# Kernel tuning notes

Hardware: AMD Instinct MI355X
Metric: run time of the kernel (lower is better)

## Reference

```python
import jax, jax.numpy as jnp
import numpy as np

H = 128
NH = 8  # num attention heads


def _ln(x, g, b, eps=1e-5):
    m = x.mean(-1, keepdims=True)
    v = ((x - m) ** 2).mean(-1, keepdims=True)
    return (x - m) / jnp.sqrt(v + eps) * g + b


def _mha(q_in, kv_in, Wqkv, bqkv, Wo, bo):
    # torch nn.MultiheadAttention with packed in_proj, batch=1, eval (no dropout)
    h = q_in.shape[-1]
    hd = h // NH
    Wq, Wk, Wv = Wqkv[:h], Wqkv[h:2 * h], Wqkv[2 * h:]
    bq, bk, bv = bqkv[:h], bqkv[h:2 * h], bqkv[2 * h:]
    q = (q_in @ Wq.T + bq).reshape(-1, NH, hd).transpose(1, 0, 2)   # [nh, Nq, hd]
    k = (kv_in @ Wk.T + bk).reshape(-1, NH, hd).transpose(1, 0, 2)  # [nh, Nk, hd]
    v = (kv_in @ Wv.T + bv).reshape(-1, NH, hd).transpose(1, 0, 2)
    scores = jnp.einsum('hqd,hkd->hqk', q, k) / jnp.sqrt(jnp.asarray(hd, q.dtype))
    attn = jax.nn.softmax(scores, axis=-1)
    out = jnp.einsum('hqk,hkd->hqd', attn, v)                       # [nh, Nq, hd]
    out = out.transpose(1, 0, 2).reshape(-1, h)
    return out @ Wo.T + bo


def setup_inputs() -> dict:
    key = jax.random.key(0)
    ks = jax.random.split(key, 32)
    s = 0.05
    d = {
        'ligand_features': jax.random.normal(ks[0], (512, 128), jnp.float32),
        'pocket_features': jax.random.normal(ks[1], (1024, 128), jnp.float32),
        'ligand_coords': jax.random.uniform(ks[2], (512, 3), jnp.float32) * 20.0,
        'pocket_coords': jax.random.uniform(ks[3], (1024, 3), jnp.float32) * 20.0,
        # projections
        'Wl': jax.random.normal(ks[4], (H, 128), jnp.float32) * s,
        'bl': jnp.zeros((H,), jnp.float32),
        'Wp': jax.random.normal(ks[5], (H, 128), jnp.float32) * s,
        'bp': jnp.zeros((H,), jnp.float32),
        # distance encoder: 1 -> h/4 -> h/2 -> h
        'Wd1': jax.random.normal(ks[6], (H // 4, 1), jnp.float32) * s,
        'bd1': jnp.zeros((H // 4,), jnp.float32),
        'Wd2': jax.random.normal(ks[7], (H // 2, H // 4), jnp.float32) * s,
        'bd2': jnp.zeros((H // 2,), jnp.float32),
        'Wd3': jax.random.normal(ks[8], (H, H // 2), jnp.float32) * s,
        'bd3': jnp.zeros((H,), jnp.float32),
        # gates
        'Wgl': jax.random.normal(ks[9], (H, 2 * H), jnp.float32) * s,
        'bgl': jnp.zeros((H,), jnp.float32),
        'Wgp': jax.random.normal(ks[10], (H, 2 * H), jnp.float32) * s,
        'bgp': jnp.zeros((H,), jnp.float32),
        # shared cross-attention (packed qkv like torch)
        'Wqkv': jax.random.normal(ks[11], (3 * H, H), jnp.float32) * s,
        'bqkv': jnp.zeros((3 * H,), jnp.float32),
        'Wo': jax.random.normal(ks[12], (H, H), jnp.float32) * s,
        'bo': jnp.zeros((H,), jnp.float32),
        # layer norms
        'g_l': jnp.ones((H,), jnp.float32),
        'be_l': jnp.zeros((H,), jnp.float32),
        'g_p': jnp.ones((H,), jnp.float32),
        'be_p': jnp.zeros((H,), jnp.float32),
    }
    return d


def reference(ligand_features, pocket_features, ligand_coords, pocket_coords,
              Wl, bl, Wp, bp, Wd1, bd1, Wd2, bd2, Wd3, bd3,
              Wgl, bgl, Wgp, bgp, Wqkv, bqkv, Wo, bo,
              g_l, be_l, g_p, be_p):
    lig = ligand_features @ Wl.T + bl   # [Nl, H]
    poc = pocket_features @ Wp.T + bp   # [Np, H]

    # pairwise distances [Nl, Np]
    diff = ligand_coords[:, None, :] - pocket_coords[None, :, :]
    dist = jnp.sqrt(jnp.sum(diff * diff, axis=-1))

    # distance encoder MLP applied elementwise -> [Nl, Np, H]
    e = jax.nn.relu(dist[..., None] @ Wd1.T + bd1)
    e = jax.nn.relu(e @ Wd2.T + bd2)
    enc = e @ Wd3.T + bd3
    m = enc.mean(axis=-1)               # [Nl, Np]

    # ligand enhancement: softmax over pocket axis
    sw_l = jax.nn.softmax(-m, axis=-1)          # [Nl, Np]
    agg_l = sw_l @ poc                          # [Nl, H]
    gate_l = jax.nn.sigmoid(jnp.concatenate([lig, agg_l], axis=-1) @ Wgl.T + bgl)
    lig_enh = gate_l * lig + (1.0 - gate_l) * agg_l

    # pocket enhancement: transposed encoding, softmax over ligand axis
    sw_p = jax.nn.softmax(-m.T, axis=-1)        # [Np, Nl]
    agg_p = sw_p @ lig                          # [Np, H]
    gate_p = jax.nn.sigmoid(jnp.concatenate([poc, agg_p], axis=-1) @ Wgp.T + bgp)
    poc_enh = gate_p * poc + (1.0 - gate_p) * agg_p

    lig_att = _mha(lig_enh, poc_enh, Wqkv, bqkv, Wo, bo)
    poc_att = _mha(poc_enh, lig_enh, Wqkv, bqkv, Wo, bo)

    lig_fused = _ln(lig_enh + lig_att, g_l, be_l)
    poc_fused = _ln(poc_enh + poc_att, g_p, be_p)
    return (lig_fused, poc_fused)
```

## Files before the change

### kernel.cpp

```cpp
#include <hip/hip_runtime.h>
#include <math.h>

#define NL 512
#define NP 1024
#define HDIM 128

#define TAB_N 8192
#define DMAX 34.65f

#define M_OFF    128
#define WLT_OFF  (M_OFF)
#define WPT_OFF  (M_OFF + 16384)
#define WQT_OFF  (M_OFF + 32768)
#define WOT_OFF  (M_OFF + 81920)
#define WGLT_OFF (M_OFF + 98304)
#define WGPT_OFF (M_OFF + 131072)
#define TAB_OFF  (M_OFF + 163840)
#define LIG_OFF  (M_OFF + NL*NP)
#define POC_OFF  (LIG_OFF + NL*HDIM)
#define LENH_OFF (POC_OFF + NP*HDIM)
#define PENH_OFF (LENH_OFF + NL*HDIM)
#define QKVL_OFF (PENH_OFF + NP*HDIM)
#define QKVP_OFF (QKVL_OFF + NL*384)
#define PARTL_OFF (QKVP_OFF + NP*384)
#define PARTP_OFF (PARTL_OFF + 512*8*8*18)

__device__ __forceinline__ float dot4f(float4 a, float4 b){
  return fmaf(a.x,b.x, fmaf(a.y,b.y, fmaf(a.z,b.z, a.w*b.w)));
}

__device__ __forceinline__ void tpose(const float* __restrict__ src, float* __restrict__ dst,
                                      int O, int K, int blk0, int t){
  int e0 = blk0*1024 + t*4;
  #pragma unroll
  for (int i = 0; i < 4; i++){
    int e = e0 + i;
    int o = e / K, k = e - o*K;
    dst[(size_t)k*O + o] = src[(size_t)o*K + k];
  }
}
__global__ __launch_bounds__(256) void prep_all(const float* __restrict__ Wl, const float* __restrict__ Wp,
                                                const float* __restrict__ Wqkv, const float* __restrict__ Wo,
                                                const float* __restrict__ Wgl, const float* __restrict__ Wgp,
                                                const float* __restrict__ Wd1, const float* __restrict__ bd1,
                                                const float* __restrict__ Wd2, const float* __restrict__ bd2,
                                                const float* __restrict__ Wd3, const float* __restrict__ bd3,
                                                float* __restrict__ ws){
  int b = blockIdx.x, t = threadIdx.x;
  if (b < 160){
    if      (b < 16)  tpose(Wl,   ws + WLT_OFF,  128, 128, b,       t);
    else if (b < 32)  tpose(Wp,   ws + WPT_OFF,  128, 128, b - 16,  t);
    else if (b < 80)  tpose(Wqkv, ws + WQT_OFF,  384, 128, b - 32,  t);
    else if (b < 96)  tpose(Wo,   ws + WOT_OFF,  128, 128, b - 80,  t);
    else if (b < 128) tpose(Wgl,  ws + WGLT_OFF, 128, 256, b - 96,  t);
    else              tpose(Wgp,  ws + WGPT_OFF, 128, 256, b - 128, t);
    return;
  }
  float* tab = ws + TAB_OFF;
  __shared__ float sWd1[32], sbd1[32], sWd2[2048], sbd2[64], swd3m[64];
  __shared__ float sbd3m;
  int idx = (b - 160) * 256 + t;
  if (t < 64){
    float s = 0.f;
    #pragma unroll 8
    for (int i = 0; i < 128; i++) s += Wd3[i*64 + t];
    swd3m[t] = s * (1.f/128.f);
  } else if (t == 64){
    float s = 0.f;
    for (int i = 0; i < 128; i++) s += bd3[i];
    sbd3m = s * (1.f/128.f);
  } else if (t >= 128 && t < 160){ sWd1[t-128] = Wd1[t-128]; sbd1[t-128] = bd1[t-128]; }
  else if (t >= 160 && t < 224){ sbd2[t-160] = bd2[t-160]; }
  for (int k = t; k < 2048; k += 256) sWd2[k] = Wd2[k];
  __syncthreads();

  float d = (float)idx * (DMAX / (float)(TAB_N - 1));
  float4 e1q[8];
  const float4* w1q = (const float4*)sWd1;
  const float4* b1q = (const float4*)sbd1;
  #pragma unroll
  for (int k4 = 0; k4 < 8; k4++){
    float4 w = w1q[k4], bb = b1q[k4];
    float4 e;
    e.x = fmaxf(fmaf(d, w.x, bb.x), 0.f);
    e.y = fmaxf(fmaf(d, w.y, bb.y), 0.f);
    e.z = fmaxf(fmaf(d, w.z, bb.z), 0.f);
    e.w = fmaxf(fmaf(d, w.w, bb.w), 0.f);
    e1q[k4] = e;
  }
  float mv = sbd3m;
  #pragma unroll 4
  for (int j2 = 0; j2 < 64; j2++){
    const float4* wrow = (const float4*)(sWd2 + j2*32);
    float a0 = 0.f, a1 = 0.f, a2 = 0.f, a3 = 0.f;
    #pragma unroll
    for (int k4 = 0; k4 < 8; k4++){
      float4 w = wrow[k4], e = e1q[k4];
      a0 = fmaf(w.x, e.x, a0);
      a1 = fmaf(w.y, e.y, a1);
      a2 = fmaf(w.z, e.z, a2);
      a3 = fmaf(w.w, e.w, a3);
    }
    float e2v = fmaxf(sbd2[j2] + ((a0+a1)+(a2+a3)), 0.f);
    mv = fmaf(swd3m[j2], e2v, mv);
  }
  tab[idx] = mv;
}

__global__ __launch_bounds__(1024) void proj_kernel(const float* __restrict__ lf, const float* __restrict__ pf,
                                                    const float* __restrict__ WlT, const float* __restrict__ bl,
                                                    const float* __restrict__ WpT, const float* __restrict__ bp,
                                                    float* __restrict__ lig, float* __restrict__ poc){
  int b = blockIdx.x, t = threadIdx.x;
  bool isLig = (b < 64);
  int r0 = isLig ? b*8 : (b - 64)*8;
  const float* in = (isLig ? lf : pf) + (size_t)r0*HDIM;
  const float* WT = isLig ? WlT : WpT;
  const float* bias = isLig ? bl : bp;
  float* out = (isLig ? lig : poc) + (size_t)r0*HDIM;
  __shared__ float sx[8*HDIM];
  sx[t] = in[t];
  __syncthreads();
  int r = t >> 7, col = t & 127;
  const float* xr = sx + r*HDIM;
  float acc = bias[col];
  #pragma unroll 8
  for (int k = 0; k < 128; k++) acc = fmaf(WT[k*128 + col], xr[k], acc);
  out[r*HDIM + col] = acc;
}

__global__ __launch_bounds__(1024) void agg_gate_fused(const float* __restrict__ lc, const float* __restrict__ pc,
                                                       const float* __restrict__ tab,
                                                       const float* __restrict__ lig, const float* __restrict__ poc,
                                                       const float* __restrict__ WglT, const float* __restrict__ bgl,
                                                       const float* __restrict__ WgpT, const float* __restrict__ bgp,
                                                       const float* __restrict__ WqkvT, const float* __restrict__ bqkv,
                                                       float* __restrict__ lenh, float* __restrict__ penh,
                                                       float* __restrict__ qkvl, float* __restrict__ qkvp){
  int b = blockIdx.x, t = threadIdx.x;
  bool isLig = (b < NL/4);
  int r0 = isLig ? b*4 : (b - NL/4)*4;
  int n = isLig ? NP : NL;
  const float* myFeat = isLig ? lig : poc;
  const float* otherFeat = isLig ? poc : lig;
  const float* myC = isLig ? lc : pc;
  const float* otC = isLig ? pc : lc;

  __shared__ float w[4*NP];
  __shared__ float sx[4*HDIM];
  __shared__ float sa[4*HDIM];
  __shared__ float part[16*512];
  __shared__ float redm[16];
  __shared__ float sgm[4], sinv[4];

  int rr = t >> 8, u = t & 255;
  int lane = t & 63, wv = t >> 6;
  int row = r0 + rr;

  if (t < 512) sx[t] = myFeat[(size_t)r0*HDIM + t];

  float cx = myC[row*3+0], cy = myC[row*3+1], cz = myC[row*3+2];
  const float inv_h = (float)(TAB_N - 1) / DMAX;
  int per = n >> 8;

  float xs[4];
  float lmax = -1e30f;
  for (int k = 0; k < per; k++){
    int j = u + (k << 8);
    float ox = otC[j*3+0], oy = otC[j*3+1], oz = otC[j*3+2];
    float dx = cx-ox, dy = cy-oy, dz = cz-oz;
    float d = sqrtf(fmaf(dx,dx, fmaf(dy,dy, dz*dz)));
    float xf = d * inv_h;
    int i0 = (int)xf;
    i0 = (i0 > TAB_N-2) ? (TAB_N-2) : i0;
    float f = xf - (float)i0;
    float v0 = tab[i0], v1 = tab[i0+1];
    xs[k] = -fmaf(f, v1 - v0, v0);
    lmax = fmaxf(lmax, xs[k]);
  }
  float v = lmax;
  #pragma unroll
  for (int off = 32; off; off >>= 1) v = fmaxf(v, __shfl_down(v, off));
  if (lane == 0) redm[wv] = v;
  __syncthreads();
  if (t < 4) sgm[t] = fmaxf(fmaxf(redm[t*4+0], redm[t*4+1]), fmaxf(redm[t*4+2], redm[t*4+3]));
  __syncthreads();
  float gm = sgm[rr];
  float lsum = 0.f;
  for (int k = 0; k < per; k++){
    float e = __expf(xs[k] - gm);
    w[rr*NP + u + (k << 8)] = e;
    lsum += e;
  }
  v = lsum;
  #pragma unroll
  for (int off = 32; off; off >>= 1) v += __shfl_down(v, off);
  if (lane == 0) redm[wv] = v;
  __syncthreads();
  if (t < 4) sinv[t] = 1.0f / ((redm[t*4+0] + redm[t*4+1]) + (redm[t*4+2] + redm[t*4+3]));
  __syncthreads();

  {
    int jg = t >> 6;
    int rp = (t >> 5) & 1;
    int c4 = t & 31;
    int per2 = n >> 4;
    int jb0 = jg * per2;
    int rA = rp*2, rB = rp*2 + 1;
    const float4* of4 = (const float4*)otherFeat;
    const float* wA = w + rA*NP;
    const float* wB = w + rB*NP;
    float4 accA = {0,0,0,0}, accB = {0,0,0,0};
    #pragma unroll 4
    for (int jj = 0; jj < per2; jj++){
      int j = jb0 + jj;
      float4 f = of4[(size_t)j*32 + c4];
      float w0 = wA[j], w1 = wB[j];
      accA.x = fmaf(w0, f.x, accA.x); accA.y = fmaf(w0, f.y, accA.y);
      accA.z = fmaf(w0, f.z, accA.z); accA.w = fmaf(w0, f.w, accA.w);
      accB.x = fmaf(w1, f.x, accB.x); accB.y = fmaf(w1, f.y, accB.y);
      accB.z = fmaf(w1, f.z, accB.z); accB.w = fmaf(w1, f.w, accB.w);
    }
    float4* p4 = (float4*)part;
    p4[jg*128 + rA*32 + c4] = accA;
    p4[jg*128 + rB*32 + c4] = accB;
  }
  __syncthreads();
  {
    float4* p4 = (float4*)part;
    #pragma unroll
    for (int s = 8; s >= 1; s >>= 1){
      if (t < s*128){
        int jg2 = t >> 7, rem = t & 127;
        float4 a = p4[jg2*128 + rem], bb = p4[(jg2+s)*128 + rem];
        a.x += bb.x; a.y += bb.y; a.z += bb.z; a.w += bb.w;
        p4[jg2*128 + rem] = a;
      }
      __syncthreads();
    }
  }
  if (t < 512){
    int r = t >> 7;
    sa[t] = part[t] * sinv[r];
  }
  __syncthreads();

  float enh_val = 0.f;
  {
    if (t < 512){
      int r = t >> 7, col = t & 127;
      const float* WT = isLig ? WglT : WgpT;
      const float* bg = isLig ? bgl : bgp;
      const float* xr = sx + r*HDIM;
      const float* ar = sa + r*HDIM;
      float g = bg[col];
      #pragma unroll 8
      for (int k = 0; k < 128; k++) g = fmaf(WT[k*128 + col], xr[k], g);
      #pragma unroll 8
      for (int k = 0; k < 128; k++) g = fmaf(WT[(128+k)*128 + col], ar[k], g);
      g = 1.0f / (1.0f + __expf(-g));
      float xv = xr[col], av = ar[col];
      enh_val = fmaf(g, xv - av, av);
      float* dst = isLig ? (lenh + (size_t)(r0+r)*HDIM) : (penh + (size_t)(r0+r)*HDIM);
      dst[col] = enh_val;
    }
  }
  __syncthreads();
  if (t < 512) sa[t] = enh_val;
  __syncthreads();

  if (t < 512){
    int r = t >> 7, c0 = t & 127;
    const float* er = sa + r*HDIM;
    float acc0 = bqkv[c0], acc1 = bqkv[c0+128], acc2 = bqkv[c0+256];
    #pragma unroll 4
    for (int k = 0; k < 128; k++){
      float xv = er[k];
      const float* wk = WqkvT + k*384;
      acc0 = fmaf(wk[c0],       xv, acc0);
      acc1 = fmaf(wk[c0+128],   xv, acc1);
      acc2 = fmaf(wk[c0+256],   xv, acc2);
    }
    float* qout = (isLig ? qkvl : qkvp) + (size_t)(r0+r)*384;
    qout[c0] = acc0; qout[c0+128] = acc1; qout[c0+256] = acc2;
  }
}

__global__ __launch_bounds__(256) void attn_part(const float* __restrict__ qkvl, const float* __restrict__ qkvp,
                                                 float* __restrict__ partL, float* __restrict__ partP){
  int bx = blockIdx.x;
  int t = threadIdx.x;
  const float* qsrc; const float* kvsrc; int qt, slice; bool isLig;
  if (bx < 256){ isLig = true;  qt = bx >> 3; slice = bx & 7; qsrc = qkvl; kvsrc = qkvp; }
  else { int b2 = bx - 256; isLig = false; qt = b2 >> 2; slice = b2 & 3; qsrc = qkvp; kvsrc = qkvl; }
  int g = t >> 6, tt = t & 63;
  int h = tt >> 3, qp = tt & 7;
  int j0 = slice*128 + g*32;

  const float4* qA = (const float4*)(qsrc + (size_t)(qt*16+qp)*384 + h*16);
  const float4* qB = (const float4*)(qsrc + (size_t)(qt*16+qp+8)*384 + h*16);
  float4 a0 = qA[0], a1 = qA[1], a2 = qA[2], a3 = qA[3];
  float4 b0 = qB[0], b1 = qB[1], b2 = qB[2], b3 = qB[3];
  float mA = -1e30f, lA = 0.f, mB = -1e30f, lB = 0.f;
  float4 OA0={0,0,0,0}, OA1={0,0,0,0}, OA2={0,0,0,0}, OA3={0,0,0,0};
  float4 OB0={0,0,0,0}, OB1={0,0,0,0}, OB2={0,0,0,0}, OB3={0,0,0,0};

  __shared__ float sKV[8192];
  float* myKV = sKV + g*2048;

  for (int tile = 0; tile < 4; tile++){
    int jbase = j0 + tile*8;
    __syncthreads();
    #pragma unroll
    for (int nn = 0; nn < 8; nn++){
      int v4 = tt + nn*64;
      int jj = v4 >> 6, c4 = v4 & 63;
      ((float4*)myKV)[jj*64 + c4] = *(const float4*)(kvsrc + (size_t)(jbase+jj)*384 + 128 + c4*4);
    }
    __syncthreads();
    float sA[8], sB[8];
    #pragma unroll
    for (int jj = 0; jj < 8; jj++){
      const float4* kk = (const float4*)(myKV + jj*256 + h*16);
      float4 k0 = kk[0], k1 = kk[1], k2 = kk[2], k3 = kk[3];
      sA[jj] = (dot4f(a0,k0) + dot4f(a1,k1) + dot4f(a2,k2) + dot4f(a3,k3)) * 0.25f;
      sB[jj] = (dot4f(b0,k0) + dot4f(b1,k1) + dot4f(b2,k2) + dot4f(b3,k3)) * 0.25f;
    }
    float mtA = sA[0], mtB = sB[0];
    #pragma unroll
    for (int jj = 1; jj < 8; jj++){ mtA = fmaxf(mtA, sA[jj]); mtB = fmaxf(mtB, sB[jj]); }
    float mnA = fmaxf(mA, mtA), mnB = fmaxf(mB, mtB);
    float cA = __expf(mA - mnA), cB = __expf(mB - mnB);
    lA *= cA; lB *= cB;
    OA0.x*=cA; OA0.y*=cA; OA0.z*=cA; OA0.w*=cA;
    OA1.x*=cA; OA1.y*=cA; OA1.z*=cA; OA1.w*=cA;
    OA2.x*=cA; OA2.y*=cA; OA2.z*=cA; OA2.w*=cA;
    OA3.x*=cA; OA3.y*=cA; OA3.z*=cA; OA3.w*=cA;
    OB0.x*=cB; OB0.y*=cB; OB0.z*=cB; OB0.w*=cB;
    OB1.x*=cB; OB1.y*=cB; OB1.z*=cB; OB1.w*=cB;
    OB2.x*=cB; OB2.y*=cB; OB2.z*=cB; OB2.w*=cB;
    OB3.x*=cB; OB3.y*=cB; OB3.z*=cB; OB3.w*=cB;
    #pragma unroll
    for (int jj = 0; jj < 8; jj++){
      float pA = __expf(sA[jj] - mnA);
      float pB = __expf(sB[jj] - mnB);
      lA += pA; lB += pB;
      const float4* vv = (const float4*)(myKV + jj*256 + 128 + h*16);
      float4 v0 = vv[0], v1 = vv[1], v2 = vv[2], v3 = vv[3];
      OA0.x = fmaf(pA, v0.x, OA0.x); OA0.y = fmaf(pA, v0.y, OA0.y);
      OA0.z = fmaf(pA, v0.z, OA0.z); OA0.w = fmaf(pA, v0.w, OA0.w);
      OA1.x = fmaf(pA, v1.x, OA1.x); OA1.y = fmaf(pA, v1.y, OA1.y);
      OA1.z = fmaf(pA, v1.z, OA1.z); OA1.w = fmaf(pA, v1.w, OA1.w);
      OA2.x = fmaf(pA, v2.x, OA2.x); OA2.y = fmaf(pA, v2.y, OA2.y);
      OA2.z = fmaf(pA, v2.z, OA2.z); OA2.w = fmaf(pA, v2.w, OA2.w);
      OA3.x = fmaf(pA, v3.x, OA3.x); OA3.y = fmaf(pA, v3.y, OA3.y);
      OA3.z = fmaf(pA, v3.z, OA3.z); OA3.w = fmaf(pA, v3.w, OA3.w);
      OB0.x = fmaf(pB, v0.x, OB0.x); OB0.y = fmaf(pB, v0.y, OB0.y);
      OB0.z = fmaf(pB, v0.z, OB0.z); OB0.w = fmaf(pB, v0.w, OB0.w);
      OB1.x = fmaf(pB, v1.x, OB1.x); OB1.y = fmaf(pB, v1.y, OB1.y);
      OB1.z = fmaf(pB, v1.z, OB1.z); OB1.w = fmaf(pB, v1.w, OB1.w);
      OB2.x = fmaf(pB, v2.x, OB2.x); OB2.y = fmaf(pB, v2.y, OB2.y);
      OB2.z = fmaf(pB, v2.z, OB2.z); OB2.w = fmaf(pB, v2.w, OB2.w);
      OB3.x = fmaf(pB, v3.x, OB3.x); OB3.y = fmaf(pB, v3.y, OB3.y);
      OB3.z = fmaf(pB, v3.z, OB3.z); OB3.w = fmaf(pB, v3.w, OB3.w);
    }
    mA = mnA; mB = mnB;
  }

  __syncthreads();
  if (g > 0){
    float* bA = sKV + (size_t)((g-1)*128 + tt*2)*19;
    bA[0]=mA; bA[1]=lA;
    bA[2]=OA0.x; bA[3]=OA0.y; bA[4]=OA0.z; bA[5]=OA0.w;
    bA[6]=OA1.x; bA[7]=OA1.y; bA[8]=OA1.z; bA[9]=OA1.w;
    bA[10]=OA2.x; bA[11]=OA2.y; bA[12]=OA2.z; bA[13]=OA2.w;
    bA[14]=OA3.x; bA[15]=OA3.y; bA[16]=OA3.z; bA[17]=OA3.w;
    float* bB = bA + 19;
    bB[0]=mB; bB[1]=lB;
    bB[2]=OB0.x; bB[3]=OB0.y; bB[4]=OB0.z; bB[5]=OB0.w;
    bB[6]=OB1.x; bB[7]=OB1.y; bB[8]=OB1.z; bB[9]=OB1.w;
    bB[10]=OB2.x; bB[11]=OB2.y; bB[12]=OB2.z; bB[13]=OB2.w;
    bB[14]=OB3.x; bB[15]=OB3.y; bB[16]=OB3.z; bB[17]=OB3.w;
  }
  __syncthreads();
  if (g == 0){
    float M = mA, L = lA;
    float O[16] = {OA0.x,OA0.y,OA0.z,OA0.w, OA1.x,OA1.y,OA1.z,OA1.w,
                   OA2.x,OA2.y,OA2.z,OA2.w, OA3.x,OA3.y,OA3.z,OA3.w};
    #pragma unroll
    for (int gg = 1; gg < 4; gg++){
      const float* br = sKV + (size_t)((gg-1)*128 + tt*2)*19;
      float m1 = br[0], l1 = br[1];
      float Mn = fmaxf(M, m1);
      float e0 = __expf(M - Mn), e1 = __expf(m1 - Mn);
      L = L*e0 + l1*e1;
      #pragma unroll
      for (int k = 0; k < 16; k++) O[k] = O[k]*e0 + br[2+k]*e1;
      M = Mn;
    }
    int rowA = qt*16 + qp;
    float* dst = isLig ? (partL + ((size_t)(rowA*8 + h)*8 + slice)*18)
                       : (partP + ((size_t)(rowA*8 + h)*4 + slice)*18);
    dst[0] = M; dst[1] = L;
    #pragma unroll
    for (int k = 0; k < 16; k++) dst[2+k] = O[k];
    M = mB; L = lB;
    float Ob[16] = {OB0.x,OB0.y,OB0.z,OB0.w, OB1.x,OB1.y,OB1.z,OB1.w,
                    OB2.x,OB2.y,OB2.z,OB2.w, OB3.x,OB3.y,OB3.z,OB3.w};
    #pragma unroll
    for (int gg = 1; gg < 4; gg++){
      const float* br = sKV + (size_t)((gg-1)*128 + tt*2 + 1)*19;
      float m1 = br[0], l1 = br[1];
      float Mn = fmaxf(M, m1);
      float e0 = __expf(M - Mn), e1 = __expf(m1 - Mn);
      L = L*e0 + l1*e1;
      #pragma unroll
      for (int k = 0; k < 16; k++) Ob[k] = Ob[k]*e0 + br[2+k]*e1;
      M = Mn;
    }
    int rowB = qt*16 + qp + 8;
    float* dstB = isLig ? (partL + ((size_t)(rowB*8 + h)*8 + slice)*18)
                        : (partP + ((size_t)(rowB*8 + h)*4 + slice)*18);
    dstB[0] = M; dstB[1] = L;
    #pragma unroll
    for (int k = 0; k < 16; k++) dstB[2+k] = Ob[k];
  }
}

__global__ __launch_bounds__(1024) void merge_ln(const float* __restrict__ partL, const float* __restrict__ partP,
                                                 const float* __restrict__ lenh, const float* __restrict__ penh,
                                                 const float* __restrict__ WoT, const float* __restrict__ bo,
                                                 const float* __restrict__ g_l, const float* __restrict__ be_l,
                                                 const float* __restrict__ g_p, const float* __restrict__ be_p,
                                                 float* __restrict__ out){
  int b = blockIdx.x, t = threadIdx.x;
  int r0 = b*8;
  int r = t >> 7, c = t & 127;
  int gr = r0 + r;
  int h = c >> 4, cc = c & 15;
  int ns; const float* base;
  if (gr < NL){ ns = 8; base = partL + ((size_t)(gr*8 + h))*8*18; }
  else        { ns = 4; base = partP + ((size_t)((gr-NL)*8 + h))*4*18; }
  float M = -1e30f;
  for (int s = 0; s < ns; s++) M = fmaxf(M, base[s*18]);
  float Lsum = 0.f, Osum = 0.f;
  for (int s = 0; s < ns; s++){
    float e = __expf(base[s*18] - M);
    Lsum = fmaf(e, base[s*18+1], Lsum);
    Osum = fmaf(e, base[s*18+2+cc], Osum);
  }
  __shared__ float sAtt[8*HDIM];
  sAtt[t] = Osum / Lsum;
  __syncthreads();
  float o = bo[c];
  const float* sA = sAtt + r*HDIM;
  #pragma unroll 8
  for (int k = 0; k < 128; k++) o = fmaf(WoT[k*128 + c], sA[k], o);
  const float* enh = (gr < NL) ? (lenh + (size_t)gr*HDIM) : (penh + (size_t)(gr-NL)*HDIM);
  float x = enh[c] + o;
  __shared__ float sred[32];
  int wid = t >> 6;
  float v = x;
  #pragma unroll
  for (int off = 32; off; off >>= 1) v += __shfl_down(v, off);
  if ((t & 63) == 0) sred[wid] = v;
  __syncthreads();
  float mu = (sred[2*r] + sred[2*r+1]) * (1.f/128.f);
  float dx = x - mu;
  v = dx*dx;
  #pragma unroll
  for (int off = 32; off; off >>= 1) v += __shfl_down(v, off);
  if ((t & 63) == 0) sred[16 + wid] = v;
  __syncthreads();
  float var = (sred[16 + 2*r] + sred[16 + 2*r+1]) * (1.f/128.f);
  float y = dx * rsqrtf(var + 1e-5f);
  if (gr < NL) y = fmaf(y, g_l[c], be_l[c]);
  else         y = fmaf(y, g_p[c], be_p[c]);
  out[(size_t)gr*HDIM + c] = y;
}

extern "C" void kernel_launch(void* const* d_in, const int* in_sizes, int n_in,
                              void* d_out, int out_size, void* d_ws, size_t ws_size,
                              hipStream_t stream){
  const float* lf   = (const float*)d_in[0];
  const float* pf   = (const float*)d_in[1];
  const float* lc   = (const float*)d_in[2];
  const float* pc   = (const float*)d_in[3];
  const float* Wl   = (const float*)d_in[4];
  const float* bl   = (const float*)d_in[5];
  const float* Wp   = (const float*)d_in[6];
  const float* bp   = (const float*)d_in[7];
  const float* Wd1  = (const float*)d_in[8];
  const float* bd1  = (const float*)d_in[9];
  const float* Wd2  = (const float*)d_in[10];
  const float* bd2  = (const float*)d_in[11];
  const float* Wd3  = (const float*)d_in[12];
  const float* bd3  = (const float*)d_in[13];
  const float* Wgl  = (const float*)d_in[14];
  const float* bgl  = (const float*)d_in[15];
  const float* Wgp  = (const float*)d_in[16];
  const float* bgp  = (const float*)d_in[17];
  const float* Wqkv = (const float*)d_in[18];
  const float* bqkv = (const float*)d_in[19];
  const float* Wo   = (const float*)d_in[20];
  const float* bo   = (const float*)d_in[21];
  const float* g_l  = (const float*)d_in[22];
  const float* be_l = (const float*)d_in[23];
  const float* g_p  = (const float*)d_in[24];
  const float* be_p = (const float*)d_in[25];

  float* ws  = (float*)d_ws;
  float* out = (float*)d_out;
  float* lig   = ws + LIG_OFF;
  float* poc   = ws + POC_OFF;
  float* lenh  = ws + LENH_OFF;
  float* penh  = ws + PENH_OFF;
  float* qkvl  = ws + QKVL_OFF;
  float* qkvp  = ws + QKVP_OFF;
  float* partL = ws + PARTL_OFF;
  float* partP = ws + PARTP_OFF;
  float* tab   = ws + TAB_OFF;

  prep_all<<<192, 256, 0, stream>>>(Wl, Wp, Wqkv, Wo, Wgl, Wgp, Wd1, bd1, Wd2, bd2, Wd3, bd3, ws);
  proj_kernel<<<192, 1024, 0, stream>>>(lf, pf, ws + WLT_OFF, bl, ws + WPT_OFF, bp, lig, poc);
  agg_gate_fused<<<NL/4 + NP/4, 1024, 0, stream>>>(lc, pc, tab, lig, poc,
                                                   ws + WGLT_OFF, bgl, ws + WGPT_OFF, bgp,
                                                   ws + WQT_OFF, bqkv,
                                                   lenh, penh, qkvl, qkvp);
  attn_part<<<512, 256, 0, stream>>>(qkvl, qkvp, partL, partP);
  merge_ln<<<192, 1024, 0, stream>>>(partL, partP, lenh, penh, ws + WOT_OFF, bo,
                                     g_l, be_l, g_p, be_p, out);
}
```

Before: 198.1 us.

## Shrink per-block row counts to launch more, smaller blocks across kernels

Three kernels (projection, aggregation/gate, merge+layernorm) now handle 2 rows per block instead of 4 or 8, using smaller thread blocks (256/512) and more blocks (768). Inside agg_gate_fused the work is remapped: the gate matvec splits its two K halves across thread groups and adds the partials in shared memory, and the QKV projection splits its three output columns across all threads. The aim is to fill more CUs on the MI355X and raise occupancy. The cost is more reloading of the weight matrices per row and extra block overhead.

```diff
diff --git a/kernel.cpp b/kernel.cpp
--- a/kernel.cpp
+++ b/kernel.cpp
@@ -107,18 +107,18 @@
   tab[idx] = mv;
 }
 
-__global__ __launch_bounds__(1024) void proj_kernel(const float* __restrict__ lf, const float* __restrict__ pf,
-                                                    const float* __restrict__ WlT, const float* __restrict__ bl,
-                                                    const float* __restrict__ WpT, const float* __restrict__ bp,
-                                                    float* __restrict__ lig, float* __restrict__ poc){
+__global__ __launch_bounds__(256) void proj_kernel(const float* __restrict__ lf, const float* __restrict__ pf,
+                                                   const float* __restrict__ WlT, const float* __restrict__ bl,
+                                                   const float* __restrict__ WpT, const float* __restrict__ bp,
+                                                   float* __restrict__ lig, float* __restrict__ poc){
   int b = blockIdx.x, t = threadIdx.x;
-  bool isLig = (b < 64);
-  int r0 = isLig ? b*8 : (b - 64)*8;
+  bool isLig = (b < NL/2);
+  int r0 = isLig ? b*2 : (b - NL/2)*2;
   const float* in = (isLig ? lf : pf) + (size_t)r0*HDIM;
   const float* WT = isLig ? WlT : WpT;
   const float* bias = isLig ? bl : bp;
   float* out = (isLig ? lig : poc) + (size_t)r0*HDIM;
-  __shared__ float sx[8*HDIM];
+  __shared__ float sx[2*HDIM];
   sx[t] = in[t];
   __syncthreads();
   int r = t >> 7, col = t & 127;
@@ -129,35 +129,36 @@
   out[r*HDIM + col] = acc;
 }
 
-__global__ __launch_bounds__(1024) void agg_gate_fused(const float* __restrict__ lc, const float* __restrict__ pc,
-                                                       const float* __restrict__ tab,
-                                                       const float* __restrict__ lig, const float* __restrict__ poc,
-                                                       const float* __restrict__ WglT, const float* __restrict__ bgl,
-                                                       const float* __restrict__ WgpT, const float* __restrict__ bgp,
-                                                       const float* __restrict__ WqkvT, const float* __restrict__ bqkv,
-                                                       float* __restrict__ lenh, float* __restrict__ penh,
-                                                       float* __restrict__ qkvl, float* __restrict__ qkvp){
+__global__ __launch_bounds__(512) void agg_gate_fused(const float* __restrict__ lc, const float* __restrict__ pc,
+                                                      const float* __restrict__ tab,
+                                                      const float* __restrict__ lig, const float* __restrict__ poc,
+                                                      const float* __restrict__ WglT, const float* __restrict__ bgl,
+                                                      const float* __restrict__ WgpT, const float* __restrict__ bgp,
+                                                      const float* __restrict__ WqkvT, const float* __restrict__ bqkv,
+                                                      float* __restrict__ lenh, float* __restrict__ penh,
+                                                      float* __restrict__ qkvl, float* __restrict__ qkvp){
   int b = blockIdx.x, t = threadIdx.x;
-  bool isLig = (b < NL/4);
-  int r0 = isLig ? b*4 : (b - NL/4)*4;
+  bool isLig = (b < NL/2);
+  int r0 = isLig ? b*2 : (b - NL/2)*2;
   int n = isLig ? NP : NL;
   const float* myFeat = isLig ? lig : poc;
   const float* otherFeat = isLig ? poc : lig;
   const float* myC = isLig ? lc : pc;
   const float* otC = isLig ? pc : lc;
 
-  __shared__ float w[4*NP];
-  __shared__ float sx[4*HDIM];
-  __shared__ float sa[4*HDIM];
-  __shared__ float part[16*512];
-  __shared__ float redm[16];
-  __shared__ float sgm[4], sinv[4];
+  __shared__ float w[2*NP];
+  __shared__ float sx[2*HDIM];
+  __shared__ float sa[2*HDIM];
+  __shared__ float4 part4[8*64];
+  __shared__ float gpart[512];
+  __shared__ float redm[8];
+  __shared__ float sgm[2], sinv[2];
 
   int rr = t >> 8, u = t & 255;
   int lane = t & 63, wv = t >> 6;
   int row = r0 + rr;
 
-  if (t < 512) sx[t] = myFeat[(size_t)r0*HDIM + t];
+  if (t < 256) sx[t] = myFeat[(size_t)r0*HDIM + t];
 
   float cx = myC[row*3+0], cy = myC[row*3+1], cz = myC[row*3+2];
   const float inv_h = (float)(TAB_N - 1) / DMAX;
@@ -183,7 +184,7 @@
   for (int off = 32; off; off >>= 1) v = fmaxf(v, __shfl_down(v, off));
   if (lane == 0) redm[wv] = v;
   __syncthreads();
-  if (t < 4) sgm[t] = fmaxf(fmaxf(redm[t*4+0], redm[t*4+1]), fmaxf(redm[t*4+2], redm[t*4+3]));
+  if (t < 2) sgm[t] = fmaxf(fmaxf(redm[t*4+0], redm[t*4+1]), fmaxf(redm[t*4+2], redm[t*4+3]));
   __syncthreads();
   float gm = sgm[rr];
   float lsum = 0.f;
@@ -197,92 +198,90 @@
   for (int off = 32; off; off >>= 1) v += __shfl_down(v, off);
   if (lane == 0) redm[wv] = v;
   __syncthreads();
-  if (t < 4) sinv[t] = 1.0f / ((redm[t*4+0] + redm[t*4+1]) + (redm[t*4+2] + redm[t*4+3]));
+  if (t < 2) sinv[t] = 1.0f / ((redm[t*4+0] + redm[t*4+1]) + (redm[t*4+2] + redm[t*4+3]));
   __syncthreads();
 
   {
     int jg = t >> 6;
-    int rp = (t >> 5) & 1;
+    int r  = (t >> 5) & 1;
     int c4 = t & 31;
-    int per2 = n >> 4;
+    int per2 = n >> 3;
     int jb0 = jg * per2;
-    int rA = rp*2, rB = rp*2 + 1;
     const float4* of4 = (const float4*)otherFeat;
-    const float* wA = w + rA*NP;
-    const float* wB = w + rB*NP;
-    float4 accA = {0,0,0,0}, accB = {0,0,0,0};
+    const float* wR = w + r*NP;
+    float4 acc = {0,0,0,0};
     #pragma unroll 4
     for (int jj = 0; jj < per2; jj++){
       int j = jb0 + jj;
       float4 f = of4[(size_t)j*32 + c4];
-      float w0 = wA[j], w1 = wB[j];
-      accA.x = fmaf(w0, f.x, accA.x); accA.y = fmaf(w0, f.y, accA.y);
-      accA.z = fmaf(w0, f.z, accA.z); accA.w = fmaf(w0, f.w, accA.w);
-      accB.x = fmaf(w1, f.x, accB.x); accB.y = fmaf(w1, f.y, accB.y);
-      accB.z = fmaf(w1, f.z, accB.z); accB.w = fmaf(w1, f.w, accB.w);
-    }
-    float4* p4 = (float4*)part;
-    p4[jg*128 + rA*32 + c4] = accA;
-    p4[jg*128 + rB*32 + c4] = accB;
-  }
-  __syncthreads();
+      float ww = wR[j];
+      acc.x = fmaf(ww, f.x, acc.x); acc.y = fmaf(ww, f.y, acc.y);
+      acc.z = fmaf(ww, f.z, acc.z); acc.w = fmaf(ww, f.w, acc.w);
+    }
+    part4[(jg*2 + r)*32 + c4] = acc;
+  }
+  __syncthreads();
+  #pragma unroll
+  for (int s = 4; s >= 1; s >>= 1){
+    if (t < s*64){
+      int g2 = t >> 6, rem = t & 63;
+      float4 a = part4[g2*64 + rem], bb = part4[(g2+s)*64 + rem];
+      a.x += bb.x; a.y += bb.y; a.z += bb.z; a.w += bb.w;
+      part4[g2*64 + rem] = a;
+    }
+    __syncthreads();
+  }
+  if (t < 256) sa[t] = ((const float*)part4)[t] * sinv[t >> 7];
+  __syncthreads();
+
   {
-    float4* p4 = (float4*)part;
-    #pragma unroll
-    for (int s = 8; s >= 1; s >>= 1){
-      if (t < s*128){
-        int jg2 = t >> 7, rem = t & 127;
-        float4 a = p4[jg2*128 + rem], bb = p4[(jg2+s)*128 + rem];
-        a.x += bb.x; a.y += bb.y; a.z += bb.z; a.w += bb.w;
-        p4[jg2*128 + rem] = a;
+    int r  = t >> 8;
+    int kg = (t >> 7) & 1;
+    int col = t & 127;
+    const float* WT = isLig ? WglT : WgpT;
+    const float* inq = (kg == 0) ? (sx + r*HDIM) : (sa + r*HDIM);
+    const float* wbase = WT + (size_t)kg*128*128;
+    float g = 0.f;
+    #pragma unroll 8
+    for (int k = 0; k < 128; k++) g = fmaf(wbase[k*128 + col], inq[k], g);
+    gpart[kg*256 + r*128 + col] = g;
+  }
+  __syncthreads();
+  float enh_val = 0.f;
+  if (t < 256){
+    int r = t >> 7, col = t & 127;
+    const float* bg = isLig ? bgl : bgp;
+    float g = bg[col] + gpart[t] + gpart[256 + t];
+    g = 1.0f / (1.0f + __expf(-g));
+    float xv = sx[t], av = sa[t];
+    enh_val = fmaf(g, xv - av, av);
+    float* dst = isLig ? (lenh + (size_t)(r0+r)*HDIM) : (penh + (size_t)(r0+r)*HDIM);
+    dst[col] = enh_val;
+  }
+  __syncthreads();
+  if (t < 256) sa[t] = enh_val;
+  __syncthreads();
+
+  {
+    int r = t >> 8, ln = t & 255;
+    const float* er = sa + r*HDIM;
+    float* qout = (isLig ? qkvl : qkvp) + (size_t)(r0+r)*384;
+    if (ln < 128){
+      float a0 = bqkv[ln], a2 = bqkv[ln+256];
+      #pragma unroll 4
+      for (int k = 0; k < 128; k++){
+        float xv = er[k];
+        const float* wk = WqkvT + k*384;
+        a0 = fmaf(wk[ln],     xv, a0);
+        a2 = fmaf(wk[ln+256], xv, a2);
       }
-      __syncthreads();
-    }
-  }
-  if (t < 512){
-    int r = t >> 7;
-    sa[t] = part[t] * sinv[r];
-  }
-  __syncthreads();
-
-  float enh_val = 0.f;
-  {
-    if (t < 512){
-      int r = t >> 7, col = t & 127;
-      const float* WT = isLig ? WglT : WgpT;
-      const float* bg = isLig ? bgl : bgp;
-      const float* xr = sx + r*HDIM;
-      const float* ar = sa + r*HDIM;
-      float g = bg[col];
-      #pragma unroll 8
-      for (int k = 0; k < 128; k++) g = fmaf(WT[k*128 + col], xr[k], g);
-      #pragma unroll 8
-      for (int k = 0; k < 128; k++) g = fmaf(WT[(128+k)*128 + col], ar[k], g);
-      g = 1.0f / (1.0f + __expf(-g));
-      float xv = xr[col], av = ar[col];
-      enh_val = fmaf(g, xv - av, av);
-      float* dst = isLig ? (lenh + (size_t)(r0+r)*HDIM) : (penh + (size_t)(r0+r)*HDIM);
-      dst[col] = enh_val;
-    }
-  }
-  __syncthreads();
-  if (t < 512) sa[t] = enh_val;
-  __syncthreads();
-
-  if (t < 512){
-    int r = t >> 7, c0 = t & 127;
-    const float* er = sa + r*HDIM;
-    float acc0 = bqkv[c0], acc1 = bqkv[c0+128], acc2 = bqkv[c0+256];
-    #pragma unroll 4
-    for (int k = 0; k < 128; k++){
-      float xv = er[k];
-      const float* wk = WqkvT + k*384;
-      acc0 = fmaf(wk[c0],       xv, acc0);
-      acc1 = fmaf(wk[c0+128],   xv, acc1);
-      acc2 = fmaf(wk[c0+256],   xv, acc2);
-    }
-    float* qout = (isLig ? qkvl : qkvp) + (size_t)(r0+r)*384;
-    qout[c0] = acc0; qout[c0+128] = acc1; qout[c0+256] = acc2;
+      qout[ln] = a0; qout[ln+256] = a2;
+    } else {
+      float a1 = bqkv[ln];
+      #pragma unroll 4
+      for (int k = 0; k < 128; k++) a1 = fmaf(WqkvT[k*384 + ln], er[k], a1);
+      qout[ln] = a1;
+    }
   }
 }
 
@@ -427,14 +426,14 @@
   }
 }
 
-__global__ __launch_bounds__(1024) void merge_ln(const float* __restrict__ partL, const float* __restrict__ partP,
-                                                 const float* __restrict__ lenh, const float* __restrict__ penh,
-                                                 const float* __restrict__ WoT, const float* __restrict__ bo,
-                                                 const float* __restrict__ g_l, const float* __restrict__ be_l,
-                                                 const float* __restrict__ g_p, const float* __restrict__ be_p,
-                                                 float* __restrict__ out){
+__global__ __launch_bounds__(256) void merge_ln(const float* __restrict__ partL, const float* __restrict__ partP,
+                                                const float* __restrict__ lenh, const float* __restrict__ penh,
+                                                const float* __restrict__ WoT, const float* __restrict__ bo,
+                                                const float* __restrict__ g_l, const float* __restrict__ be_l,
+                                                const float* __restrict__ g_p, const float* __restrict__ be_p,
+                                                float* __restrict__ out){
   int b = blockIdx.x, t = threadIdx.x;
-  int r0 = b*8;
+  int r0 = b*2;
   int r = t >> 7, c = t & 127;
   int gr = r0 + r;
   int h = c >> 4, cc = c & 15;
@@ -449,7 +448,7 @@
     Lsum = fmaf(e, base[s*18+1], Lsum);
     Osum = fmaf(e, base[s*18+2+cc], Osum);
   }
-  __shared__ float sAtt[8*HDIM];
+  __shared__ float sAtt[2*HDIM];
   sAtt[t] = Osum / Lsum;
   __syncthreads();
   float o = bo[c];
@@ -458,7 +457,7 @@
   for (int k = 0; k < 128; k++) o = fmaf(WoT[k*128 + c], sA[k], o);
   const float* enh = (gr < NL) ? (lenh + (size_t)gr*HDIM) : (penh + (size_t)(gr-NL)*HDIM);
   float x = enh[c] + o;
-  __shared__ float sred[32];
+  __shared__ float sred[8];
   int wid = t >> 6;
   float v = x;
   #pragma unroll
@@ -470,9 +469,9 @@
   v = dx*dx;
   #pragma unroll
   for (int off = 32; off; off >>= 1) v += __shfl_down(v, off);
-  if ((t & 63) == 0) sred[16 + wid] = v;
-  __syncthreads();
-  float var = (sred[16 + 2*r] + sred[16 + 2*r+1]) * (1.f/128.f);
+  if ((t & 63) == 0) sred[4 + wid] = v;
+  __syncthreads();
+  float var = (sred[4 + 2*r] + sred[4 + 2*r+1]) * (1.f/128.f);
   float y = dx * rsqrtf(var + 1e-5f);
   if (gr < NL) y = fmaf(y, g_l[c], be_l[c]);
   else         y = fmaf(y, g_p[c], be_p[c]);
@@ -522,12 +521,12 @@
   float* tab   = ws + TAB_OFF;
 
   prep_all<<<192, 256, 0, stream>>>(Wl, Wp, Wqkv, Wo, Wgl, Wgp, Wd1, bd1, Wd2, bd2, Wd3, bd3, ws);
-  proj_kernel<<<192, 1024, 0, stream>>>(lf, pf, ws + WLT_OFF, bl, ws + WPT_OFF, bp, lig, poc);
-  agg_gate_fused<<<NL/4 + NP/4, 1024, 0, stream>>>(lc, pc, tab, lig, poc,
-                                                   ws + WGLT_OFF, bgl, ws + WGPT_OFF, bgp,
-                                                   ws + WQT_OFF, bqkv,
-                                                   lenh, penh, qkvl, qkvp);
+  proj_kernel<<<NL/2 + NP/2, 256, 0, stream>>>(lf, pf, ws + WLT_OFF, bl, ws + WPT_OFF, bp, lig, poc);
+  agg_gate_fused<<<NL/2 + NP/2, 512, 0, stream>>>(lc, pc, tab, lig, poc,
+                                                  ws + WGLT_OFF, bgl, ws + WGPT_OFF, bgp,
+                                                  ws + WQT_OFF, bqkv,
+                                                  lenh, penh, qkvl, qkvp);
   attn_part<<<512, 256, 0, stream>>>(qkvl, qkvp, partL, partP);
-  merge_ln<<<192, 1024, 0, stream>>>(partL, partP, lenh, penh, ws + WOT_OFF, bo,
-                                     g_l, be_l, g_p, be_p, out);
-}
+  merge_ln<<<NL/2 + NP/2, 256, 0, stream>>>(partL, partP, lenh, penh, ws + WOT_OFF, bo,
+                                            g_l, be_l, g_p, be_p, out);
+}
```

New measurement: 194.1 us (median of 2 runs). 2.0% less time.
